# Kernel optimization log

Hardware: AMD Instinct MI355X
Metric: run time of the kernel (lower is better)

The kernel has to match this reference:

```python
import jax, jax.numpy as jnp
import numpy as np

INPUT_DIM1 = 512
INPUT_DIM2 = 512
OUTPUT_DIM = 8192


def _make_sketch(seed_h, seed_s, input_dim, output_dim):
    # Faithful to torch module: dense [input_dim, output_dim] matrix with one
    # nonzero (+-1) per row at column rand_h[i].
    np.random.seed(seed_h)
    rand_h = np.random.randint(output_dim, size=input_dim)
    np.random.seed(seed_s)
    rand_s = (2 * np.random.randint(2, size=input_dim) - 1).astype(np.float32)
    M = np.zeros((input_dim, output_dim), dtype=np.float32)
    M[np.arange(input_dim), rand_h] = rand_s
    return jnp.asarray(M)


def setup_inputs() -> dict:
    key = jax.random.key(0)
    k1, k2 = jax.random.split(key)
    bottom1 = jax.random.normal(k1, (32, INPUT_DIM1, 14, 14), dtype=jnp.float32)
    bottom2 = jax.random.normal(k2, (32, INPUT_DIM2, 14, 14), dtype=jnp.float32)
    S1 = _make_sketch(1, 3, INPUT_DIM1, OUTPUT_DIM)
    S2 = _make_sketch(5, 7, INPUT_DIM2, OUTPUT_DIM)
    return {"bottom1": bottom1, "bottom2": bottom2, "S1": S1, "S2": S2}


def reference(bottom1, bottom2, S1, S2):
    B, _, H, W = bottom1.shape
    d = S1.shape[1]
    # [B, C, H, W] -> [B*H*W, C]
    b1 = jnp.transpose(bottom1, (0, 2, 3, 1)).reshape(-1, bottom1.shape[1])
    b2 = jnp.transpose(bottom2, (0, 2, 3, 1)).reshape(-1, bottom2.shape[1])
    sketch1 = b1 @ S1  # [N, d]
    sketch2 = b2 @ S2
    fft1 = jnp.fft.fft(sketch1, axis=-1)
    fft2 = jnp.fft.fft(sketch2, axis=-1)
    cbp_flat = jnp.real(jnp.fft.ifft(fft1 * fft2, axis=-1))
    cbp = cbp_flat.reshape(B, H, W, d)
    return cbp.sum(axis=(1, 2))  # sum_pool=True -> [B, d]
```

## Files before the change

### kernel.cpp

```cpp
#include <hip/hip_runtime.h>


#define D     8192
#define DMASK 8191
#define C     512
#define HW    196
#define NB    32
#define LDK   40
#define NCH   7
#define NSL   16

typedef __attribute__((ext_vector_type(8))) short bf16x8;
typedef __attribute__((ext_vector_type(4))) float f32x4;

__device__ __forceinline__ unsigned short f2bf(float f, unsigned xm) {
    unsigned u = __float_as_uint(f) ^ xm;
    return (unsigned short)((u + 0x7fffu + ((u >> 16) & 1u)) >> 16);
}

__global__ __launch_bounds__(256) void extract2(
    const float* __restrict__ S1, const float* __restrict__ S2,
    int* __restrict__ h1, float* __restrict__ s1,
    int* __restrict__ h2, float* __restrict__ s2)
{
    const int  row = blockIdx.x & 511;
    const bool first = blockIdx.x < 512;
    const float* S = first ? S1 : S2;
    int*   h = first ? h1 : h2;
    float* s = first ? s1 : s2;

    const float4* rp = (const float4*)(S + (size_t)row * D);
    float4 v[8];
    #pragma unroll
    for (int ii = 0; ii < 8; ++ii) v[ii] = rp[threadIdx.x + 256 * ii];

    #pragma unroll
    for (int ii = 0; ii < 8; ++ii) {
        const int base = 4 * (threadIdx.x + 256 * ii);
        if (v[ii].x != 0.f) { h[row] = base + 0; s[row] = v[ii].x; }
        if (v[ii].y != 0.f) { h[row] = base + 1; s[row] = v[ii].y; }
        if (v[ii].z != 0.f) { h[row] = base + 2; s[row] = v[ii].z; }
        if (v[ii].w != 0.f) { h[row] = base + 3; s[row] = v[ii].w; }
    }
}

__global__ __launch_bounds__(256, 2) void cbp_mfma(
    const float* __restrict__ b1, const float* __restrict__ b2,
    const int* __restrict__ h1, const float* __restrict__ s1,
    const int* __restrict__ h2, const float* __restrict__ s2,
    float* __restrict__ P)
{
    const int b  = blockIdx.z;
    const int t1 = blockIdx.y;
    const int t2 = blockIdx.x;

    __shared__ float hist[D];
    __shared__ __align__(16) unsigned short As[128 * LDK];
    __shared__ __align__(16) unsigned short Bs[128 * LDK];
    __shared__ int h1t[128], h2t[128];

    const int tid = threadIdx.x;

    #pragma unroll
    for (int i = 0; i < 8; ++i) {
        float4 z = {0.f, 0.f, 0.f, 0.f};
        ((float4*)hist)[tid + 256 * i] = z;
    }
    if (tid < 128) {
        h1t[tid] = h1[t1 * 128 + tid];
        h2t[tid] = h2[t2 * 128 + tid];
    }

    const int rr  = tid >> 3;
    const int kq4 = (tid & 7) * 4;

    const float* Abase = b1 + ((size_t)b * C + (size_t)t1 * 128) * HW;
    const float* Bbase = b2 + ((size_t)b * C + (size_t)t2 * 128) * HW;

    unsigned am[4], bm[4];
    #pragma unroll
    for (int ii = 0; ii < 4; ++ii) {
        am[ii] = (s1[t1 * 128 + rr + 32 * ii] < 0.f) ? 0x80000000u : 0u;
        bm[ii] = (s2[t2 * 128 + rr + 32 * ii] < 0.f) ? 0x80000000u : 0u;
    }

    float4 pva[4], pvb[4];
    #pragma unroll
    for (int ii = 0; ii < 4; ++ii) {
        pva[ii] = *(const float4*)(Abase + (size_t)(rr + 32 * ii) * HW + kq4);
        pvb[ii] = *(const float4*)(Bbase + (size_t)(rr + 32 * ii) * HW + kq4);
    }

    const int lane  = tid & 63;
    const int w     = tid >> 6;
    const int ln15  = lane & 15;
    const int qd    = lane >> 4;
    const int koff  = qd * 8;
    const int mbase = (w >> 1) * 64;
    const int nbase = (w & 1) * 64;

    f32x4 acc[4][4] = {};

    for (int ch = 0; ch < NCH; ++ch) {
        #pragma unroll
        for (int ii = 0; ii < 4; ++ii) {
            const int r = rr + 32 * ii;
            uint2 pa, pb;
            pa.x = (unsigned)f2bf(pva[ii].x, am[ii]) |
                   ((unsigned)f2bf(pva[ii].y, am[ii]) << 16);
            pa.y = (unsigned)f2bf(pva[ii].z, am[ii]) |
                   ((unsigned)f2bf(pva[ii].w, am[ii]) << 16);
            pb.x = (unsigned)f2bf(pvb[ii].x, bm[ii]) |
                   ((unsigned)f2bf(pvb[ii].y, bm[ii]) << 16);
            pb.y = (unsigned)f2bf(pvb[ii].z, bm[ii]) |
                   ((unsigned)f2bf(pvb[ii].w, bm[ii]) << 16);
            *(uint2*)&As[r * LDK + kq4] = pa;
            *(uint2*)&Bs[r * LDK + kq4] = pb;
        }
        __syncthreads();

        if (ch + 1 < NCH) {
            const int gk = (ch + 1) * 32 + kq4;
            const bool valid = (gk + 4 <= HW);
            const float4 z = {0.f, 0.f, 0.f, 0.f};
            #pragma unroll
            for (int ii = 0; ii < 4; ++ii) {
                pva[ii] = valid ? *(const float4*)(Abase + (size_t)(rr + 32 * ii) * HW + gk) : z;
                pvb[ii] = valid ? *(const float4*)(Bbase + (size_t)(rr + 32 * ii) * HW + gk) : z;
            }
        }

        bf16x8 av[4], bv[4];
        #pragma unroll
        for (int i = 0; i < 4; ++i)
            av[i] = *(const bf16x8*)&As[(mbase + i * 16 + ln15) * LDK + koff];
        #pragma unroll
        for (int j = 0; j < 4; ++j)
            bv[j] = *(const bf16x8*)&Bs[(nbase + j * 16 + ln15) * LDK + koff];
        #pragma unroll
        for (int i = 0; i < 4; ++i)
            #pragma unroll
            for (int j = 0; j < 4; ++j)
                acc[i][j] = __builtin_amdgcn_mfma_f32_16x16x32_bf16(
                    av[i], bv[j], acc[i][j], 0, 0, 0);
        __syncthreads();
    }

    int p1v[16];
    #pragma unroll
    for (int i = 0; i < 4; ++i)
        #pragma unroll
        for (int qq = 0; qq < 4; ++qq)
            p1v[i * 4 + qq] = h1t[mbase + i * 16 + qd * 4 + qq];
    int p2v[4];
    #pragma unroll
    for (int j = 0; j < 4; ++j)
        p2v[j] = h2t[nbase + j * 16 + ln15];

    #pragma unroll
    for (int i = 0; i < 4; ++i)
        #pragma unroll
        for (int j = 0; j < 4; ++j)
            #pragma unroll
            for (int qq = 0; qq < 4; ++qq)
                atomicAdd(&hist[(p1v[i * 4 + qq] + p2v[j]) & DMASK], acc[i][j][qq]);

    __syncthreads();

    float* Pslice = P + ((size_t)(b * NSL + t1 * 4 + t2)) * D;
    #pragma unroll
    for (int i = 0; i < 8; ++i)
        ((float4*)Pslice)[tid + 256 * i] = ((const float4*)hist)[tid + 256 * i];
}

__global__ __launch_bounds__(256) void reduce16(
    const float* __restrict__ P, float* __restrict__ out)
{
    const int idx4 = blockIdx.x * 256 + threadIdx.x;
    const int b    = idx4 >> 11;
    const int d4   = idx4 & 2047;

    const float4* base = (const float4*)(P + (size_t)b * NSL * D) + d4;
    float4 v[NSL];
    #pragma unroll
    for (int s = 0; s < NSL; ++s) v[s] = base[s * (D / 4)];

    float4 acc = v[0];
    #pragma unroll
    for (int s = 1; s < NSL; ++s) {
        acc.x += v[s].x; acc.y += v[s].y; acc.z += v[s].z; acc.w += v[s].w;
    }
    ((float4*)out)[idx4] = acc;
}

extern "C" void kernel_launch(void* const* d_in, const int* in_sizes, int n_in,
                              void* d_out, int out_size, void* d_ws, size_t ws_size,
                              hipStream_t stream)
{
    const float* bottom1 = (const float*)d_in[0];
    const float* bottom2 = (const float*)d_in[1];
    const float* S1      = (const float*)d_in[2];
    const float* S2      = (const float*)d_in[3];
    float* out = (float*)d_out;

    float* P  = (float*)d_ws;
    int*   h1 = (int*)(P + (size_t)NB * NSL * D);
    int*   h2 = h1 + C;
    float* s1 = (float*)(h2 + C);
    float* s2 = s1 + C;

    extract2<<<1024, 256, 0, stream>>>(S1, S2, h1, s1, h2, s2);
    cbp_mfma<<<dim3(4, 4, NB), 256, 0, stream>>>(bottom1, bottom2,
                                                 h1, s1, h2, s2, P);
    reduce16<<<256, 256, 0, stream>>>(P, out);
}
```

Measured before the change: 152.9 us.

## Load MFMA operands directly from global into registers, skip LDS staging

Measured after the change: 163.2 us. +6.7%, slower.

```diff
diff --git a/kernel.cpp b/kernel.cpp
--- a/kernel.cpp
+++ b/kernel.cpp
@@ -6,16 +6,24 @@
 #define C     512
 #define HW    196
 #define NB    32
-#define LDK   40
 #define NCH   7
 #define NSL   16
 
 typedef __attribute__((ext_vector_type(8))) short bf16x8;
 typedef __attribute__((ext_vector_type(4))) float f32x4;
 
-__device__ __forceinline__ unsigned short f2bf(float f, unsigned xm) {
-    unsigned u = __float_as_uint(f) ^ xm;
+__device__ __forceinline__ unsigned short f2bf(float f) {
+    unsigned u = __float_as_uint(f);
     return (unsigned short)((u + 0x7fffu + ((u >> 16) & 1u)) >> 16);
+}
+
+__device__ __forceinline__ bf16x8 pack8(float4 a, float4 b) {
+    bf16x8 r;
+    r[0] = (short)f2bf(a.x); r[1] = (short)f2bf(a.y);
+    r[2] = (short)f2bf(a.z); r[3] = (short)f2bf(a.w);
+    r[4] = (short)f2bf(b.x); r[5] = (short)f2bf(b.y);
+    r[6] = (short)f2bf(b.z); r[7] = (short)f2bf(b.w);
+    return r;
 }
 
 __global__ __launch_bounds__(256) void extract2(
@@ -23,24 +31,37 @@
     int* __restrict__ h1, float* __restrict__ s1,
     int* __restrict__ h2, float* __restrict__ s2)
 {
-    const int  row = blockIdx.x & 511;
+    const int  row   = blockIdx.x & 511;
     const bool first = blockIdx.x < 512;
     const float* S = first ? S1 : S2;
-    int*   h = first ? h1 : h2;
-    float* s = first ? s1 : s2;
-
     const float4* rp = (const float4*)(S + (size_t)row * D);
+    const int tid = threadIdx.x;
+
     float4 v[8];
     #pragma unroll
-    for (int ii = 0; ii < 8; ++ii) v[ii] = rp[threadIdx.x + 256 * ii];
-
+    for (int ii = 0; ii < 8; ++ii) v[ii] = rp[tid + 256 * ii];
+
+    float ssum = 0.f, wsum = 0.f;
     #pragma unroll
     for (int ii = 0; ii < 8; ++ii) {
-        const int base = 4 * (threadIdx.x + 256 * ii);
-        if (v[ii].x != 0.f) { h[row] = base + 0; s[row] = v[ii].x; }
-        if (v[ii].y != 0.f) { h[row] = base + 1; s[row] = v[ii].y; }
-        if (v[ii].z != 0.f) { h[row] = base + 2; s[row] = v[ii].z; }
-        if (v[ii].w != 0.f) { h[row] = base + 3; s[row] = v[ii].w; }
+        const float base = (float)(4 * (tid + 256 * ii));
+        ssum += (v[ii].x + v[ii].y) + (v[ii].z + v[ii].w);
+        wsum += v[ii].x * base + v[ii].y * (base + 1.f)
+              + v[ii].z * (base + 2.f) + v[ii].w * (base + 3.f);
+    }
+    #pragma unroll
+    for (int off = 32; off; off >>= 1) {
+        ssum += __shfl_down(ssum, off, 64);
+        wsum += __shfl_down(wsum, off, 64);
+    }
+    __shared__ float rs[4], rw[4];
+    if ((tid & 63) == 0) { rs[tid >> 6] = ssum; rw[tid >> 6] = wsum; }
+    __syncthreads();
+    if (tid == 0) {
+        const float st = (rs[0] + rs[1]) + (rs[2] + rs[3]);
+        const float wt = (rw[0] + rw[1]) + (rw[2] + rw[3]);
+        if (first) { h1[row] = (int)(wt * st); s1[row] = st; }
+        else       { h2[row] = (int)(wt * st); s2[row] = st; }
     }
 }
 
@@ -55,9 +76,8 @@
     const int t2 = blockIdx.x;
 
     __shared__ float hist[D];
-    __shared__ __align__(16) unsigned short As[128 * LDK];
-    __shared__ __align__(16) unsigned short Bs[128 * LDK];
-    __shared__ int h1t[128], h2t[128];
+    __shared__ int   h1t[128], h2t[128];
+    __shared__ float s1t[128], s2t[128];
 
     const int tid = threadIdx.x;
 
@@ -67,28 +87,8 @@
         ((float4*)hist)[tid + 256 * i] = z;
     }
     if (tid < 128) {
-        h1t[tid] = h1[t1 * 128 + tid];
-        h2t[tid] = h2[t2 * 128 + tid];
-    }
-
-    const int rr  = tid >> 3;
-    const int kq4 = (tid & 7) * 4;
-
-    const float* Abase = b1 + ((size_t)b * C + (size_t)t1 * 128) * HW;
-    const float* Bbase = b2 + ((size_t)b * C + (size_t)t2 * 128) * HW;
-
-    unsigned am[4], bm[4];
-    #pragma unroll
-    for (int ii = 0; ii < 4; ++ii) {
-        am[ii] = (s1[t1 * 128 + rr + 32 * ii] < 0.f) ? 0x80000000u : 0u;
-        bm[ii] = (s2[t2 * 128 + rr + 32 * ii] < 0.f) ? 0x80000000u : 0u;
-    }
-
-    float4 pva[4], pvb[4];
-    #pragma unroll
-    for (int ii = 0; ii < 4; ++ii) {
-        pva[ii] = *(const float4*)(Abase + (size_t)(rr + 32 * ii) * HW + kq4);
-        pvb[ii] = *(const float4*)(Bbase + (size_t)(rr + 32 * ii) * HW + kq4);
+        h1t[tid] = h1[t1 * 128 + tid];  s1t[tid] = s1[t1 * 128 + tid];
+        h2t[tid] = h2[t2 * 128 + tid];  s2t[tid] = s2[t2 * 128 + tid];
     }
 
     const int lane  = tid & 63;
@@ -99,75 +99,86 @@
     const int mbase = (w >> 1) * 64;
     const int nbase = (w & 1) * 64;
 
+    const float* Ap[4];
+    const float* Bp[4];
+    #pragma unroll
+    for (int i = 0; i < 4; ++i) {
+        Ap[i] = b1 + ((size_t)b * C + t1 * 128 + mbase + i * 16 + ln15) * HW + koff;
+        Bp[i] = b2 + ((size_t)b * C + t2 * 128 + nbase + i * 16 + ln15) * HW + koff;
+    }
+
     f32x4 acc[4][4] = {};
 
+    float4 la[8], lb[8];
+    #pragma unroll
+    for (int i = 0; i < 4; ++i) {
+        la[2 * i]     = *(const float4*)(Ap[i]);
+        la[2 * i + 1] = *(const float4*)(Ap[i] + 4);
+        lb[2 * i]     = *(const float4*)(Bp[i]);
+        lb[2 * i + 1] = *(const float4*)(Bp[i] + 4);
+    }
+
+    #pragma unroll
     for (int ch = 0; ch < NCH; ++ch) {
-        #pragma unroll
-        for (int ii = 0; ii < 4; ++ii) {
-            const int r = rr + 32 * ii;
-            uint2 pa, pb;
-            pa.x = (unsigned)f2bf(pva[ii].x, am[ii]) |
-                   ((unsigned)f2bf(pva[ii].y, am[ii]) << 16);
-            pa.y = (unsigned)f2bf(pva[ii].z, am[ii]) |
-                   ((unsigned)f2bf(pva[ii].w, am[ii]) << 16);
-            pb.x = (unsigned)f2bf(pvb[ii].x, bm[ii]) |
-                   ((unsigned)f2bf(pvb[ii].y, bm[ii]) << 16);
-            pb.y = (unsigned)f2bf(pvb[ii].z, bm[ii]) |
-                   ((unsigned)f2bf(pvb[ii].w, bm[ii]) << 16);
-            *(uint2*)&As[r * LDK + kq4] = pa;
-            *(uint2*)&Bs[r * LDK + kq4] = pb;
-        }
-        __syncthreads();
-
+        float4 na[8], nb[8];
         if (ch + 1 < NCH) {
-            const int gk = (ch + 1) * 32 + kq4;
-            const bool valid = (gk + 4 <= HW);
+            const int base = (ch + 1) * 32;
+            const bool v0 = (base + koff + 4) <= HW;
+            const bool v1 = (base + koff + 8) <= HW;
             const float4 z = {0.f, 0.f, 0.f, 0.f};
             #pragma unroll
-            for (int ii = 0; ii < 4; ++ii) {
-                pva[ii] = valid ? *(const float4*)(Abase + (size_t)(rr + 32 * ii) * HW + gk) : z;
-                pvb[ii] = valid ? *(const float4*)(Bbase + (size_t)(rr + 32 * ii) * HW + gk) : z;
+            for (int i = 0; i < 4; ++i) {
+                na[2 * i]     = v0 ? *(const float4*)(Ap[i] + base)     : z;
+                na[2 * i + 1] = v1 ? *(const float4*)(Ap[i] + base + 4) : z;
+                nb[2 * i]     = v0 ? *(const float4*)(Bp[i] + base)     : z;
+                nb[2 * i + 1] = v1 ? *(const float4*)(Bp[i] + base + 4) : z;
             }
         }
 
         bf16x8 av[4], bv[4];
         #pragma unroll
-        for (int i = 0; i < 4; ++i)
-            av[i] = *(const bf16x8*)&As[(mbase + i * 16 + ln15) * LDK + koff];
-        #pragma unroll
-        for (int j = 0; j < 4; ++j)
-            bv[j] = *(const bf16x8*)&Bs[(nbase + j * 16 + ln15) * LDK + koff];
+        for (int i = 0; i < 4; ++i) {
+            av[i] = pack8(la[2 * i], la[2 * i + 1]);
+            bv[i] = pack8(lb[2 * i], lb[2 * i + 1]);
+        }
         #pragma unroll
         for (int i = 0; i < 4; ++i)
             #pragma unroll
             for (int j = 0; j < 4; ++j)
                 acc[i][j] = __builtin_amdgcn_mfma_f32_16x16x32_bf16(
                     av[i], bv[j], acc[i][j], 0, 0, 0);
-        __syncthreads();
-    }
-
-    int p1v[16];
-    #pragma unroll
-    for (int i = 0; i < 4; ++i)
+
+        if (ch + 1 < NCH) {
+            #pragma unroll
+            for (int t = 0; t < 8; ++t) { la[t] = na[t]; lb[t] = nb[t]; }
+        }
+    }
+
+    __syncthreads();
+
+    int   p2v[4]; float q2[4];
+    #pragma unroll
+    for (int j = 0; j < 4; ++j) {
+        const int cc = nbase + j * 16 + ln15;
+        p2v[j] = h2t[cc];  q2[j] = s2t[cc];
+    }
+    #pragma unroll
+    for (int i = 0; i < 4; ++i) {
         #pragma unroll
-        for (int qq = 0; qq < 4; ++qq)
-            p1v[i * 4 + qq] = h1t[mbase + i * 16 + qd * 4 + qq];
-    int p2v[4];
-    #pragma unroll
-    for (int j = 0; j < 4; ++j)
-        p2v[j] = h2t[nbase + j * 16 + ln15];
-
-    #pragma unroll
-    for (int i = 0; i < 4; ++i)
-        #pragma unroll
-        for (int j = 0; j < 4; ++j)
-            #pragma unroll
-            for (int qq = 0; qq < 4; ++qq)
-                atomicAdd(&hist[(p1v[i * 4 + qq] + p2v[j]) & DMASK], acc[i][j][qq]);
+        for (int qq = 0; qq < 4; ++qq) {
+            const int rw2 = mbase + i * 16 + qd * 4 + qq;
+            const int   p1 = h1t[rw2];
+            const float sr = s1t[rw2];
+            #pragma unroll
+            for (int j = 0; j < 4; ++j)
+                atomicAdd(&hist[(p1 + p2v[j]) & DMASK],
+                          acc[i][j][qq] * sr * q2[j]);
+        }
+    }
 
     __syncthreads();
 
-    float* Pslice = P + ((size_t)(b * NSL + t1 * 4 + t2)) * D;
+    float* Pslice = P + (size_t)(b * NSL + t1 * 4 + t2) * D;
     #pragma unroll
     for (int i = 0; i < 8; ++i)
         ((float4*)Pslice)[tid + 256 * i] = ((const float4*)hist)[tid + 256 * i];
```
